# Kernel optimization log

Hardware: AMD Instinct MI355X
Metric: run time of the kernel (lower is better)

Reference implementation:

```python
import jax, jax.numpy as jnp
import numpy as np

D_MODEL, N_HEADS, D_C, D_COMP, D_ROPE = 2048, 16, 512, 768, 64
D_HEAD = D_MODEL // N_HEADS  # 128
B, S = 2, 2048
ROPE_THETA = 10000.0


def _rope_cos_sin(seq_len, dim):
    # frequencies for pairwise complex rotation, dim = per-head rope dim (even)
    inv_freq = 1.0 / (ROPE_THETA ** (jnp.arange(0, dim, 2, dtype=jnp.float32) / dim))
    t = jnp.arange(seq_len, dtype=jnp.float32)
    ang = t[:, None] * inv_freq[None, :]  # [S, dim/2]
    return jnp.cos(ang), jnp.sin(ang)


def _apply_rope(x, cos, sin):
    # x: [B, S, H, dr]; rotate consecutive pairs (view_as_complex semantics)
    x1, x2 = x[..., 0::2], x[..., 1::2]
    c = cos[None, :, None, :]
    s = sin[None, :, None, :]
    y1 = x1 * c - x2 * s
    y2 = x1 * s + x2 * c
    return jnp.stack([y1, y2], axis=-1).reshape(x.shape)


def setup_inputs() -> dict:
    key = jax.random.key(0)
    ks = jax.random.split(key, 9)
    sc = 0.02
    return {
        "x": jax.random.normal(ks[0], (B, S, D_MODEL), jnp.float32),
        "Wd": jax.random.normal(ks[1], (D_MODEL, D_C), jnp.float32) * sc,
        "bd": jnp.zeros((D_C,), jnp.float32),
        "Wu": jax.random.normal(ks[2], (D_C, N_HEADS * D_HEAD), jnp.float32) * sc,
        "bu": jnp.zeros((N_HEADS * D_HEAD,), jnp.float32),
        "Wqd": jax.random.normal(ks[3], (D_MODEL, D_COMP), jnp.float32) * sc,
        "bqd": jnp.zeros((D_COMP,), jnp.float32),
        "Wqu": jax.random.normal(ks[4], (D_COMP, N_HEADS * D_HEAD), jnp.float32) * sc,
        "bqu": jnp.zeros((N_HEADS * D_HEAD,), jnp.float32),
        "Wqr": jax.random.normal(ks[5], (D_COMP, N_HEADS * D_ROPE), jnp.float32) * sc,
        "bqr": jnp.zeros((N_HEADS * D_ROPE,), jnp.float32),
        "Wkr": jax.random.normal(ks[6], (D_MODEL, N_HEADS * D_ROPE), jnp.float32) * sc,
        "bkr": jnp.zeros((N_HEADS * D_ROPE,), jnp.float32),
        "Wo": jax.random.normal(ks[7], (N_HEADS * D_HEAD, D_MODEL), jnp.float32) * sc,
        "bo": jnp.zeros((D_MODEL,), jnp.float32),
    }


def reference(x, Wd, bd, Wu, bu, Wqd, bqd, Wqu, bqu, Wqr, bqr, Wkr, bkr, Wo, bo):
    b, s, _ = x.shape
    # low-rank KV compression
    kv_c = x @ Wd + bd                                   # [B,S,d_c]
    kv_up = (kv_c @ Wu + bu).reshape(b, s, N_HEADS, D_HEAD)  # shared K-content / V
    # low-rank Q compression
    q_cmp = x @ Wqd + bqd                                # [B,S,d_comp]
    q_c = (q_cmp @ Wqu + bqu).reshape(b, s, N_HEADS, D_HEAD)
    # decoupled RoPE branches
    cos, sin = _rope_cos_sin(s, D_ROPE)
    q_r = _apply_rope((q_cmp @ Wqr + bqr).reshape(b, s, N_HEADS, D_ROPE), cos, sin)
    k_r = _apply_rope((x @ Wkr + bkr).reshape(b, s, N_HEADS, D_ROPE), cos, sin)
    q = jnp.concatenate([q_c, q_r], axis=-1)             # [B,S,H,dh+dr]
    k = jnp.concatenate([kv_up, k_r], axis=-1)           # [B,S,H,dh+dr]
    scale = 1.0 / np.sqrt(D_HEAD).astype(np.float32)
    scores = jnp.einsum('bqhd,bkhd->bhqk', q, k) * scale  # [B,H,S,S]
    probs = jax.nn.softmax(scores, axis=-1)
    out = jnp.einsum('bhqk,bkhd->bqhd', probs, kv_up)    # v == kv_up (as in source)
    out = out.reshape(b, s, N_HEADS * D_HEAD)
    return out @ Wo + bo
```

## Files before the change

### kernel.cpp

```cpp
#include <hip/hip_runtime.h>
#include <cmath>

typedef __bf16 bf16;
typedef __bf16 bf16x8 __attribute__((ext_vector_type(8)));
typedef __bf16 bf16x4 __attribute__((ext_vector_type(4)));
typedef float f32x4 __attribute__((ext_vector_type(4)));
typedef int i32x4 __attribute__((ext_vector_type(4)));

#define S_LEN 2048
#define QK_LD 3072

__device__ __forceinline__ void async_copy16(const bf16* g, bf16* l) {
    __builtin_amdgcn_global_load_lds(
        (const __attribute__((address_space(1))) void*)g,
        (__attribute__((address_space(3))) void*)l, 16, 0, 0);
}

__global__ __launch_bounds__(256) void cast_f32_bf16(const float* __restrict__ in,
                                                     bf16* __restrict__ out) {
    size_t i = ((size_t)blockIdx.x * 256 + threadIdx.x) * 8;
    float4 a = *(const float4*)(in + i);
    float4 b = *(const float4*)(in + i + 4);
    bf16x8 v;
    v[0] = (bf16)a.x; v[1] = (bf16)a.y; v[2] = (bf16)a.z; v[3] = (bf16)a.w;
    v[4] = (bf16)b.x; v[5] = (bf16)b.y; v[6] = (bf16)b.z; v[7] = (bf16)b.w;
    *(bf16x8*)(out + i) = v;
}

struct TSeg { const float* src; bf16* dst; int K, N, blk0; };
struct TArgs { TSeg s[7]; };

__global__ __launch_bounds__(256) void transpose_all(TArgs a) {
    __shared__ float tile[64][68];
    int b = blockIdx.x, si = 0;
#pragma unroll
    for (int i = 1; i < 7; ++i) if (b >= a.s[i].blk0) si = i;
    TSeg sg = a.s[si];
    int local = b - sg.blk0;
    int kTiles = sg.K >> 6;
    int kt = local % kTiles, nt = local / kTiles;
    int k0 = kt * 64, n0 = nt * 64;
    int K = sg.K, N = sg.N;
    int t = threadIdx.x;
#pragma unroll
    for (int i = 0; i < 4; ++i) {
        int c = t + i * 256;
        int r = c >> 4, off = (c & 15) * 4;
        float4 v = *(const float4*)(sg.src + (size_t)(k0 + r) * N + n0 + off);
        tile[r][off] = v.x; tile[r][off + 1] = v.y;
        tile[r][off + 2] = v.z; tile[r][off + 3] = v.w;
    }
    __syncthreads();
#pragma unroll
    for (int i = 0; i < 2; ++i) {
        int c = t + i * 256;
        int nr = c >> 3, koff = (c & 7) * 8;
        bf16x8 v;
#pragma unroll
        for (int j = 0; j < 8; ++j) v[j] = (bf16)tile[koff + j][nr];
        *(bf16x8*)(sg.dst + (size_t)(n0 + nr) * K + k0 + koff) = v;
    }
}

__global__ __launch_bounds__(256) void setup_small(const float* __restrict__ bd,
                                                   const float* __restrict__ bqd,
                                                   const float* __restrict__ bkr,
                                                   const float* __restrict__ bqu,
                                                   const float* __restrict__ bqr,
                                                   float* __restrict__ bcat,
                                                   float2* __restrict__ tab) {
    if (blockIdx.x < 21) {
        int i = blockIdx.x * 256 + threadIdx.x;
        if (i < 512) bcat[i] = bd[i];
        else if (i < 1280) bcat[i] = bqd[i - 512];
        else if (i < 2304) bcat[i] = bkr[i - 1280];
        else if (i < 4352) bcat[i] = bqu[i - 2304];
        else if (i < 5376) bcat[i] = bqr[i - 4352];
    } else {
        int id = (blockIdx.x - 21) * 256 + threadIdx.x;
        int s = id >> 5, i = id & 31;
        float f = expf(-0.2878231366242557f * (float)i);
        float ang = (float)s * f;
        tab[id] = make_float2(cosf(ang), sinf(ang));
    }
}

__device__ __forceinline__ void gemm_core(const bf16* __restrict__ A, int lda,
                                          const bf16* __restrict__ Bt,
                                          const float* __restrict__ bias,
                                          void* __restrict__ out0,
                                          void* __restrict__ out1,
                                          int Ndim, int Kdim, int mode,
                                          const float2* __restrict__ tab,
                                          int bn, int bm, bf16* As, bf16* Bs) {
    int t = threadIdx.x;
    int w = t >> 6, lane = t & 63;
    int wm = (w >> 1) * 64, wn = (w & 1) * 64;
    int l15 = lane & 15, q4 = lane >> 4;
    f32x4 acc[4][4] = {};

    int lrow = lane >> 2;
    int lcol = (lane & 3) * 8;
    int c0 = w * 2, c1 = w * 2 + 1;
    const bf16* aS0 = A  + (size_t)(bm * 128 + c0 * 16 + lrow) * lda + lcol;
    const bf16* aS1 = A  + (size_t)(bm * 128 + c1 * 16 + lrow) * lda + lcol;
    const bf16* bS0 = Bt + (size_t)(bn * 128 + c0 * 16 + lrow) * Kdim + lcol;
    const bf16* bS1 = Bt + (size_t)(bn * 128 + c1 * 16 + lrow) * Kdim + lcol;
    bf16* aD0 = &As[c0 * 512]; bf16* aD1 = &As[c1 * 512];
    bf16* bD0 = &Bs[c0 * 512]; bf16* bD1 = &Bs[c1 * 512];

    for (int kt = 0; kt < Kdim; kt += 32) {
        async_copy16(aS0 + kt, aD0);
        async_copy16(aS1 + kt, aD1);
        async_copy16(bS0 + kt, bD0);
        async_copy16(bS1 + kt, bD1);
        __syncthreads();
        bf16x8 af[4], bfr[4];
#pragma unroll
        for (int mb = 0; mb < 4; ++mb)
            af[mb] = *(const bf16x8*)&As[(wm + mb * 16 + l15) * 32 + q4 * 8];
#pragma unroll
        for (int nb = 0; nb < 4; ++nb)
            bfr[nb] = *(const bf16x8*)&Bs[(wn + nb * 16 + l15) * 32 + q4 * 8];
#pragma unroll
        for (int mb = 0; mb < 4; ++mb)
#pragma unroll
            for (int nb = 0; nb < 4; ++nb)
                acc[mb][nb] = __builtin_amdgcn_mfma_f32_16x16x32_bf16(
                    af[mb], bfr[nb], acc[mb][nb], 0, 0, 0);
        __syncthreads();
    }

#pragma unroll
    for (int mb = 0; mb < 4; ++mb) {
        int row = bm * 128 + wm + mb * 16 + q4 * 4;
#pragma unroll
        for (int nb = 0; nb < 4; ++nb) {
            int col = bn * 128 + wn + nb * 16 + l15;
            float bv = bias[col];
            if (mode == 1) {
#pragma unroll
                for (int r = 0; r < 4; ++r)
                    ((float*)out0)[(size_t)(row + r) * Ndim + col] = acc[mb][nb][r] + bv;
            } else if (mode == 4) {
                if (col < 1280) {
#pragma unroll
                    for (int r = 0; r < 4; ++r)
                        ((bf16*)out0)[(size_t)(row + r) * 2304 + col] =
                            (bf16)(acc[mb][nb][r] + bv);
                } else {
                    int rel = col - 1280;
                    int hh = rel >> 6, idx = rel & 63, ii = idx >> 1, odd = idx & 1;
#pragma unroll
                    for (int r = 0; r < 4; ++r) {
                        float vv = acc[mb][nb][r] + bv;
                        float pp = __shfl_xor(vv, 1, 64);
                        float2 cs = tab[((row + r) & 2047) * 32 + ii];
                        float o = vv * cs.x + (odd ? pp * cs.y : -pp * cs.y);
                        ((bf16*)out1)[(size_t)(row + r) * QK_LD + hh * 192 + 128 + idx] =
                            (bf16)o;
                    }
                }
            } else if (mode == 5) {
                if (col < 2048) {
                    int hh = col >> 7, dd = col & 127;
#pragma unroll
                    for (int r = 0; r < 4; ++r)
                        ((bf16*)out0)[(size_t)(row + r) * QK_LD + hh * 192 + dd] =
                            (bf16)(acc[mb][nb][r] + bv);
                } else {
                    int rel = col - 2048;
                    int hh = rel >> 6, idx = rel & 63, ii = idx >> 1, odd = idx & 1;
#pragma unroll
                    for (int r = 0; r < 4; ++r) {
                        float vv = acc[mb][nb][r] + bv;
                        float pp = __shfl_xor(vv, 1, 64);
                        float2 cs = tab[((row + r) & 2047) * 32 + ii];
                        float o = vv * cs.x + (odd ? pp * cs.y : -pp * cs.y);
                        ((bf16*)out0)[(size_t)(row + r) * QK_LD + hh * 192 + 128 + idx] =
                            (bf16)o;
                    }
                }
            } else {
                int hh = col >> 7, dd = col & 127;
                bf16x4 pack;
#pragma unroll
                for (int r = 0; r < 4; ++r) {
                    float vv = acc[mb][nb][r] + bv;
                    ((bf16*)out0)[(size_t)(row + r) * QK_LD + hh * 192 + dd] = (bf16)vv;
                    pack[r] = (bf16)vv;
                }
                int bidx = row >> 11, srow = row & 2047;
                *(bf16x4*)((bf16*)out1 +
                           ((size_t)(bidx * 16 + hh) * 128 + dd) * S_LEN + srow) = pack;
            }
        }
    }
}

__global__ __launch_bounds__(256) void gemm_bt(const bf16* __restrict__ A, int lda,
                                               const bf16* __restrict__ Bt,
                                               const float* __restrict__ bias,
                                               void* __restrict__ out0,
                                               void* __restrict__ out1,
                                               int Ndim, int Kdim, int mode,
                                               const float2* __restrict__ tab) {
    __shared__ bf16 As[128 * 32];
    __shared__ bf16 Bs[128 * 32];
    gemm_core(A, lda, Bt, bias, out0, out1, Ndim, Kdim, mode, tab,
              blockIdx.x, blockIdx.y, As, Bs);
}

__global__ __launch_bounds__(256) void gemm_up(const bf16* __restrict__ xproj,
                                               const bf16* __restrict__ WuT,
                                               const float* __restrict__ bu,
                                               void* __restrict__ kbuf,
                                               void* __restrict__ vt,
                                               const bf16* __restrict__ W2T,
                                               const float* __restrict__ bq,
                                               void* __restrict__ qbuf,
                                               const float2* __restrict__ tab) {
    __shared__ bf16 As[128 * 32];
    __shared__ bf16 Bs[128 * 32];
    int bn = blockIdx.x;
    if (bn < 16)
        gemm_core(xproj, 2304, WuT, bu, kbuf, vt, 2048, 512, 6, tab,
                  bn, blockIdx.y, As, Bs);
    else
        gemm_core(xproj + 512, 2304, W2T, bq, qbuf, nullptr, 3072, 768, 5, tab,
                  bn - 16, blockIdx.y, As, Bs);
}

__global__ __launch_bounds__(256, 2) void attn(const bf16* __restrict__ qbuf,
                                               const bf16* __restrict__ kbuf,
                                               const bf16* __restrict__ vt,
                                               bf16* __restrict__ attnout) {
    __shared__ bf16 Ks[64 * 200];
    __shared__ bf16 Vs[128 * 72];
    __shared__ bf16 Ps[128 * 72];
    int bh = blockIdx.x;
    int qt = blockIdx.y;
    int b = bh >> 4, h = bh & 15;
    int t = threadIdx.x, w = t >> 6, lane = t & 63;
    int l15 = lane & 15, q4 = lane >> 4;
    const float scale = 0.08838834764831845f;

    bf16x8 qf[2][6];
    {
        size_t base = (size_t)(b * S_LEN + qt * 128 + w * 32) * QK_LD + h * 192;
#pragma unroll
        for (int mb = 0; mb < 2; ++mb)
#pragma unroll
            for (int c = 0; c < 6; ++c)
                qf[mb][c] = *(const bf16x8*)(qbuf + base +
                            (size_t)(mb * 16 + l15) * QK_LD + c * 32 + q4 * 8);
    }

    f32x4 oacc[2][8] = {};
    float denom[2] = {0.f, 0.f};
    const bf16* kb_base = kbuf + (size_t)b * S_LEN * QK_LD + h * 192;
    const bf16* vt_base = vt + (size_t)bh * 128 * S_LEN;

    int kr_[6], ko_[6], vd_[4], vo_[4];
#pragma unroll
    for (int i = 0; i < 6; ++i) { int c = t + (i << 8); kr_[i] = c / 24; ko_[i] = (c % 24) * 8; }
#pragma unroll
    for (int i = 0; i < 4; ++i) { int c = t + (i << 8); vd_[i] = c >> 3; vo_[i] = (c & 7) * 8; }

    i32x4 kreg[6], vreg[4];
#pragma unroll
    for (int i = 0; i < 6; ++i)
        kreg[i] = *(const i32x4*)(kb_base + (size_t)kr_[i] * QK_LD + ko_[i]);
#pragma unroll
    for (int i = 0; i < 4; ++i)
        vreg[i] = *(const i32x4*)(vt_base + (size_t)vd_[i] * S_LEN + vo_[i]);

    for (int kt = 0; kt < 32; ++kt) {
        __syncthreads();
#pragma unroll
        for (int i = 0; i < 6; ++i) *(i32x4*)&Ks[kr_[i] * 200 + ko_[i]] = kreg[i];
#pragma unroll
        for (int i = 0; i < 4; ++i) *(i32x4*)&Vs[vd_[i] * 72 + vo_[i]] = vreg[i];
        __syncthreads();
        if (kt < 31) {
#pragma unroll
            for (int i = 0; i < 6; ++i)
                kreg[i] = *(const i32x4*)(kb_base +
                          (size_t)((kt + 1) * 64 + kr_[i]) * QK_LD + ko_[i]);
#pragma unroll
            for (int i = 0; i < 4; ++i)
                vreg[i] = *(const i32x4*)(vt_base +
                          (size_t)vd_[i] * S_LEN + (kt + 1) * 64 + vo_[i]);
        }

        f32x4 sacc[2][4] = {};
#pragma unroll
        for (int c = 0; c < 6; ++c) {
#pragma unroll
            for (int nk = 0; nk < 4; ++nk) {
                bf16x8 kb = *(const bf16x8*)&Ks[(nk * 16 + l15) * 200 + c * 32 + q4 * 8];
#pragma unroll
                for (int mb = 0; mb < 2; ++mb)
                    sacc[mb][nk] = __builtin_amdgcn_mfma_f32_16x16x32_bf16(
                        kb, qf[mb][c], sacc[mb][nk], 0, 0, 0);
            }
        }

#pragma unroll
        for (int mb = 0; mb < 2; ++mb)
#pragma unroll
            for (int nk = 0; nk < 4; ++nk) {
                bf16x4 pk;
#pragma unroll
                for (int r = 0; r < 4; ++r) {
                    float p = __expf(fminf(sacc[mb][nk][r] * scale, 50.0f));
                    denom[mb] += p;
                    pk[r] = (bf16)p;
                }
                *(bf16x4*)&Ps[(w * 32 + mb * 16 + l15) * 72 + nk * 16 + q4 * 4] = pk;
            }

#pragma unroll
        for (int kc = 0; kc < 2; ++kc) {
            bf16x8 pa[2];
#pragma unroll
            for (int mb = 0; mb < 2; ++mb)
                pa[mb] = *(const bf16x8*)&Ps[(w * 32 + mb * 16 + l15) * 72 +
                                             kc * 32 + q4 * 8];
#pragma unroll
            for (int nb = 0; nb < 8; ++nb) {
                bf16x8 vb = *(const bf16x8*)&Vs[(nb * 16 + l15) * 72 + kc * 32 + q4 * 8];
#pragma unroll
                for (int mb = 0; mb < 2; ++mb)
                    oacc[mb][nb] = __builtin_amdgcn_mfma_f32_16x16x32_bf16(
                        pa[mb], vb, oacc[mb][nb], 0, 0, 0);
            }
        }
    }

#pragma unroll
    for (int mb = 0; mb < 2; ++mb) {
        denom[mb] += __shfl_xor(denom[mb], 16, 64);
        denom[mb] += __shfl_xor(denom[mb], 32, 64);
    }

#pragma unroll
    for (int mb = 0; mb < 2; ++mb)
#pragma unroll
        for (int r = 0; r < 4; ++r) {
            float dv = __shfl(denom[mb], q4 * 4 + r, 64);
            float inv = 1.0f / dv;
            int row = qt * 128 + w * 32 + mb * 16 + q4 * 4 + r;
#pragma unroll
            for (int nb = 0; nb < 8; ++nb) {
                int col = h * 128 + nb * 16 + l15;
                attnout[(size_t)(b * S_LEN + row) * 2048 + col] =
                    (bf16)(oacc[mb][nb][r] * inv);
            }
        }
}

extern "C" void kernel_launch(void* const* d_in, const int* in_sizes, int n_in,
                              void* d_out, int out_size, void* d_ws, size_t ws_size,
                              hipStream_t stream) {
    const float* x   = (const float*)d_in[0];
    const float* Wd  = (const float*)d_in[1];
    const float* bd  = (const float*)d_in[2];
    const float* Wu  = (const float*)d_in[3];
    const float* bu  = (const float*)d_in[4];
    const float* Wqd = (const float*)d_in[5];
    const float* bqd = (const float*)d_in[6];
    const float* Wqu = (const float*)d_in[7];
    const float* bqu = (const float*)d_in[8];
    const float* Wqr = (const float*)d_in[9];
    const float* bqr = (const float*)d_in[10];
    const float* Wkr = (const float*)d_in[11];
    const float* bkr = (const float*)d_in[12];
    const float* Wo  = (const float*)d_in[13];
    const float* bo  = (const float*)d_in[14];
    float* out = (float*)d_out;

    char* p = (char*)d_ws;
    auto alloc = [&](size_t n) { char* r = p; p += (n + 255) & ~(size_t)255; return r; };
    bf16* xb    = (bf16*)alloc((size_t)4096 * 2048 * 2);
    bf16* W1T   = (bf16*)alloc((size_t)2304 * 2048 * 2);
    bf16* W2T   = (bf16*)alloc((size_t)3072 * 768 * 2);
    bf16* WuT   = (bf16*)alloc((size_t)2048 * 512 * 2);
    bf16* WoT   = (bf16*)alloc((size_t)2048 * 2048 * 2);
    bf16* xproj = (bf16*)alloc((size_t)4096 * 2304 * 2);
    bf16* qbuf  = (bf16*)alloc((size_t)4096 * 3072 * 2);
    bf16* kbuf  = (bf16*)alloc((size_t)4096 * 3072 * 2);
    bf16* vt    = (bf16*)alloc((size_t)32 * 128 * 2048 * 2);
    bf16* aout  = (bf16*)alloc((size_t)4096 * 2048 * 2);
    float* bcat = (float*)alloc((size_t)5376 * 4);
    float2* tab = (float2*)alloc((size_t)65536 * 8);

    cast_f32_bf16<<<dim3(4096), dim3(256), 0, stream>>>(x, xb);

    TArgs ta;
    ta.s[0] = {Wd,  W1T,                       2048, 512,  0};
    ta.s[1] = {Wqd, W1T + (size_t)512 * 2048,  2048, 768,  256};
    ta.s[2] = {Wkr, W1T + (size_t)1280 * 2048, 2048, 1024, 640};
    ta.s[3] = {Wqu, W2T,                       768,  2048, 1152};
    ta.s[4] = {Wqr, W2T + (size_t)2048 * 768,  768,  1024, 1536};
    ta.s[5] = {Wu,  WuT,                       512,  2048, 1728};
    ta.s[6] = {Wo,  WoT,                       2048, 2048, 1984};
    transpose_all<<<dim3(3008), dim3(256), 0, stream>>>(ta);
    setup_small<<<dim3(277), dim3(256), 0, stream>>>(bd, bqd, bkr, bqu, bqr, bcat, tab);

    gemm_bt<<<dim3(18, 32), dim3(256), 0, stream>>>(xb, 2048, W1T, bcat,
                                                    xproj, kbuf, 2304, 2048, 4, tab);
    gemm_up<<<dim3(40, 32), dim3(256), 0, stream>>>(xproj, WuT, bu, kbuf, vt,
                                                    W2T, bcat + 2304, qbuf, tab);

    attn<<<dim3(32, 16), dim3(256), 0, stream>>>(qbuf, kbuf, vt, aout);

    gemm_bt<<<dim3(16, 32), dim3(256), 0, stream>>>(aout, 2048, WoT, bo,
                                                    out, nullptr, 2048, 2048, 1, tab);
}
```

Baseline: 437.4 us.

## Double-buffer attention K/V tiles, pass P via shuffles, swizzle LDS

Restructures the attention inner loop to use 32-key tiles with double-buffered LDS for K and V, so only one barrier per iteration is needed. The probability tile is now rearranged into MFMA operand layout with cross-lane shuffles instead of a round trip through shared memory. LDS layouts use XOR swizzles in place of padding to avoid bank conflicts, and MFMA sections are wrapped in s_setprio. The trade-off is twice as many loop iterations, extra shuffle instructions, and less MFMA work per barrier.

After: 435.3 us. Within noise of the previous version (-0.5%).

```diff
diff --git a/kernel.cpp b/kernel.cpp
--- a/kernel.cpp
+++ b/kernel.cpp
@@ -4,6 +4,7 @@
 typedef __bf16 bf16;
 typedef __bf16 bf16x8 __attribute__((ext_vector_type(8)));
 typedef __bf16 bf16x4 __attribute__((ext_vector_type(4)));
+typedef __bf16 bf16x2 __attribute__((ext_vector_type(2)));
 typedef float f32x4 __attribute__((ext_vector_type(4)));
 typedef int i32x4 __attribute__((ext_vector_type(4)));
 
@@ -14,6 +15,11 @@
     __builtin_amdgcn_global_load_lds(
         (const __attribute__((address_space(1))) void*)g,
         (__attribute__((address_space(3))) void*)l, 16, 0, 0);
+}
+
+__device__ __forceinline__ unsigned packbf(float a, float b) {
+    bf16x2 v; v[0] = (bf16)a; v[1] = (bf16)b;
+    return __builtin_bit_cast(unsigned, v);
 }
 
 __global__ __launch_bounds__(256) void cast_f32_bf16(const float* __restrict__ in,
@@ -235,9 +241,8 @@
                                                const bf16* __restrict__ kbuf,
                                                const bf16* __restrict__ vt,
                                                bf16* __restrict__ attnout) {
-    __shared__ bf16 Ks[64 * 200];
-    __shared__ bf16 Vs[128 * 72];
-    __shared__ bf16 Ps[128 * 72];
+    __shared__ bf16 Ks[2][32 * 192];
+    __shared__ bf16 Vs[2][128 * 32];
     int bh = blockIdx.x;
     int qt = blockIdx.y;
     int b = bh >> 4, h = bh & 15;
@@ -261,81 +266,114 @@
     const bf16* kb_base = kbuf + (size_t)b * S_LEN * QK_LD + h * 192;
     const bf16* vt_base = vt + (size_t)bh * 128 * S_LEN;
 
-    int kr_[6], ko_[6], vd_[4], vo_[4];
-#pragma unroll
-    for (int i = 0; i < 6; ++i) { int c = t + (i << 8); kr_[i] = c / 24; ko_[i] = (c % 24) * 8; }
-#pragma unroll
-    for (int i = 0; i < 4; ++i) { int c = t + (i << 8); vd_[i] = c >> 3; vo_[i] = (c & 7) * 8; }
-
-    i32x4 kreg[6], vreg[4];
-#pragma unroll
-    for (int i = 0; i < 6; ++i)
-        kreg[i] = *(const i32x4*)(kb_base + (size_t)kr_[i] * QK_LD + ko_[i]);
-#pragma unroll
-    for (int i = 0; i < 4; ++i)
-        vreg[i] = *(const i32x4*)(vt_base + (size_t)vd_[i] * S_LEN + vo_[i]);
-
-    for (int kt = 0; kt < 32; ++kt) {
-        __syncthreads();
-#pragma unroll
-        for (int i = 0; i < 6; ++i) *(i32x4*)&Ks[kr_[i] * 200 + ko_[i]] = kreg[i];
-#pragma unroll
-        for (int i = 0; i < 4; ++i) *(i32x4*)&Vs[vd_[i] * 72 + vo_[i]] = vreg[i];
-        __syncthreads();
-        if (kt < 31) {
-#pragma unroll
-            for (int i = 0; i < 6; ++i)
+    int kg_[3], kl_[3], vg_[2], vl_[2];
+#pragma unroll
+    for (int i = 0; i < 3; ++i) {
+        int c = t + (i << 8);
+        int kr = c / 24, u = c % 24;
+        kg_[i] = kr * QK_LD + u * 8;
+        kl_[i] = kr * 192 + ((u ^ (kr & 7)) << 3);
+    }
+#pragma unroll
+    for (int i = 0; i < 2; ++i) {
+        int c = t + (i << 8);
+        int vd = c >> 2, u = c & 3;
+        vg_[i] = vd * S_LEN + u * 8;
+        vl_[i] = vd * 32 + ((u ^ (vd & 3)) << 3);
+    }
+
+    int srcA = ((lane & 16) << 1) + l15;
+    int srcB = srcA + 16;
+    bool hiK = lane >= 32;
+
+    i32x4 kreg[3], vreg[2];
+#pragma unroll
+    for (int i = 0; i < 3; ++i) kreg[i] = *(const i32x4*)(kb_base + kg_[i]);
+#pragma unroll
+    for (int i = 0; i < 2; ++i) vreg[i] = *(const i32x4*)(vt_base + vg_[i]);
+#pragma unroll
+    for (int i = 0; i < 3; ++i) *(i32x4*)&Ks[0][kl_[i]] = kreg[i];
+#pragma unroll
+    for (int i = 0; i < 2; ++i) *(i32x4*)&Vs[0][vl_[i]] = vreg[i];
+    __syncthreads();
+
+    int cur = 0;
+    for (int kt = 0; kt < 64; ++kt) {
+        if (kt < 63) {
+#pragma unroll
+            for (int i = 0; i < 3; ++i)
                 kreg[i] = *(const i32x4*)(kb_base +
-                          (size_t)((kt + 1) * 64 + kr_[i]) * QK_LD + ko_[i]);
-#pragma unroll
-            for (int i = 0; i < 4; ++i)
-                vreg[i] = *(const i32x4*)(vt_base +
-                          (size_t)vd_[i] * S_LEN + (kt + 1) * 64 + vo_[i]);
-        }
-
-        f32x4 sacc[2][4] = {};
+                          (size_t)(kt + 1) * 32 * QK_LD + kg_[i]);
+#pragma unroll
+            for (int i = 0; i < 2; ++i)
+                vreg[i] = *(const i32x4*)(vt_base + (kt + 1) * 32 + vg_[i]);
+        }
+
+        f32x4 sacc[2][2] = {};
+        __builtin_amdgcn_s_setprio(1);
 #pragma unroll
         for (int c = 0; c < 6; ++c) {
 #pragma unroll
-            for (int nk = 0; nk < 4; ++nk) {
-                bf16x8 kb = *(const bf16x8*)&Ks[(nk * 16 + l15) * 200 + c * 32 + q4 * 8];
+            for (int nk = 0; nk < 2; ++nk) {
+                bf16x8 kb = *(const bf16x8*)&Ks[cur][(nk * 16 + l15) * 192 +
+                              (((c * 4 + q4) ^ (l15 & 7)) << 3)];
 #pragma unroll
                 for (int mb = 0; mb < 2; ++mb)
                     sacc[mb][nk] = __builtin_amdgcn_mfma_f32_16x16x32_bf16(
                         kb, qf[mb][c], sacc[mb][nk], 0, 0, 0);
             }
         }
-
-#pragma unroll
-        for (int mb = 0; mb < 2; ++mb)
-#pragma unroll
-            for (int nk = 0; nk < 4; ++nk) {
-                bf16x4 pk;
+        __builtin_amdgcn_s_setprio(0);
+
+        bf16x8 paf[2];
+#pragma unroll
+        for (int mb = 0; mb < 2; ++mb) {
+            unsigned pk[2][2];
+#pragma unroll
+            for (int nk = 0; nk < 2; ++nk) {
+                float e[4];
 #pragma unroll
                 for (int r = 0; r < 4; ++r) {
-                    float p = __expf(fminf(sacc[mb][nk][r] * scale, 50.0f));
-                    denom[mb] += p;
-                    pk[r] = (bf16)p;
+                    e[r] = __expf(fminf(sacc[mb][nk][r] * scale, 50.0f));
+                    denom[mb] += e[r];
                 }
-                *(bf16x4*)&Ps[(w * 32 + mb * 16 + l15) * 72 + nk * 16 + q4 * 4] = pk;
+                pk[nk][0] = packbf(e[0], e[1]);
+                pk[nk][1] = packbf(e[2], e[3]);
             }
-
-#pragma unroll
-        for (int kc = 0; kc < 2; ++kc) {
-            bf16x8 pa[2];
+            unsigned d[4];
+#pragma unroll
+            for (int p = 0; p < 4; ++p) {
+                int sl = (p & 2) ? srcB : srcA;
+                unsigned va = (unsigned)__shfl((int)pk[0][p & 1], sl, 64);
+                unsigned vb = (unsigned)__shfl((int)pk[1][p & 1], sl, 64);
+                d[p] = hiK ? vb : va;
+            }
+            i32x4 di;
+            di[0] = (int)d[0]; di[1] = (int)d[1];
+            di[2] = (int)d[2]; di[3] = (int)d[3];
+            paf[mb] = __builtin_bit_cast(bf16x8, di);
+        }
+
+        __builtin_amdgcn_s_setprio(1);
+#pragma unroll
+        for (int nb = 0; nb < 8; ++nb) {
+            bf16x8 vb = *(const bf16x8*)&Vs[cur][(nb * 16 + l15) * 32 +
+                          ((q4 ^ (l15 & 3)) << 3)];
 #pragma unroll
             for (int mb = 0; mb < 2; ++mb)
-                pa[mb] = *(const bf16x8*)&Ps[(w * 32 + mb * 16 + l15) * 72 +
-                                             kc * 32 + q4 * 8];
-#pragma unroll
-            for (int nb = 0; nb < 8; ++nb) {
-                bf16x8 vb = *(const bf16x8*)&Vs[(nb * 16 + l15) * 72 + kc * 32 + q4 * 8];
-#pragma unroll
-                for (int mb = 0; mb < 2; ++mb)
-                    oacc[mb][nb] = __builtin_amdgcn_mfma_f32_16x16x32_bf16(
-                        pa[mb], vb, oacc[mb][nb], 0, 0, 0);
-            }
-        }
+                oacc[mb][nb] = __builtin_amdgcn_mfma_f32_16x16x32_bf16(
+                    paf[mb], vb, oacc[mb][nb], 0, 0, 0);
+        }
+        __builtin_amdgcn_s_setprio(0);
+
+        if (kt < 63) {
+#pragma unroll
+            for (int i = 0; i < 3; ++i) *(i32x4*)&Ks[cur ^ 1][kl_[i]] = kreg[i];
+#pragma unroll
+            for (int i = 0; i < 2; ++i) *(i32x4*)&Vs[cur ^ 1][vl_[i]] = vreg[i];
+        }
+        __syncthreads();
+        cur ^= 1;
     }
 
 #pragma unroll
```
